# Performance work log

Hardware: AMD Instinct MI355X
Metric: run time of the kernel (lower is better)

## Reference

```python
import jax, jax.numpy as jnp
import numpy as np

IN_FEATURES = 8
OUT_FEATURES = 64
UNI_DEG = 3
INT_DEG = 3
N_ROWS = 500000


def _exponents():
    # Replicates the torch module's comb construction + filtering.
    deg = np.arange(UNI_DEG + 1)
    comb = np.array(np.meshgrid(*([deg] * IN_FEATURES))).T.reshape(-1, IN_FEATURES)
    s = comb.sum(axis=1)
    nz = (comb != 0).sum(axis=1)
    keep = ((nz == 1) & (s <= UNI_DEG)) | ((nz > 1) & (s <= INT_DEG))
    return comb[keep].astype(np.int32)  # [T, F] exponent matrix, T = 164


_E = _exponents()
NUM_TERMS = _E.shape[0]  # 164


def setup_inputs() -> dict:
    key = jax.random.key(0)
    kx, kw, kb = jax.random.split(key, 3)
    x = jax.random.normal(kx, (N_ROWS, IN_FEATURES), dtype=jnp.float32)
    weight = jax.random.normal(kw, (OUT_FEATURES, NUM_TERMS), dtype=jnp.float32) / np.sqrt(NUM_TERMS).astype(np.float32)
    bias = jax.random.normal(kb, (OUT_FEATURES,), dtype=jnp.float32) * 0.01
    return {"x": x, "weight": weight, "bias": bias}


def _poly_basis(x):
    # Power table pows[n, f, d] = x[n, f] ** d for d in 0..UNI_DEG.
    # Built with cumprod (exact integer powers, safe for negative x).
    xr = jnp.repeat(x[..., None], UNI_DEG, axis=-1)           # [N, F, UNI_DEG]
    pows = jnp.concatenate(
        [jnp.ones_like(x)[..., None], jnp.cumprod(xr, axis=-1)], axis=-1
    )                                                          # [N, F, UNI_DEG+1]
    E = jnp.asarray(_E)                                        # [T, F] int32
    basis = jnp.ones((x.shape[0], NUM_TERMS), x.dtype)
    for f in range(IN_FEATURES):  # small fixed loop over features
        basis = basis * pows[:, f, :][:, E[:, f]]              # gather -> [N, T]
    return basis


def reference(x, weight, bias):
    basis = _poly_basis(x)                                     # [N, T]
    return basis @ weight.T + bias                             # [N, out_features]
```

## Files before the change

kernel.cpp:

```cpp
#include <hip/hip_runtime.h>

#define NUM_ROWS 500000
#define TERMS 164
#define KSTEPS 6
#define NFRAG (KSTEPS * 4)
#define NITER ((NUM_ROWS + 63) / 64)
#define SOSTRIDE 68

typedef __attribute__((ext_vector_type(8))) short bf16x8;
typedef __attribute__((ext_vector_type(4))) float f32x4;
typedef __attribute__((ext_vector_type(4))) unsigned int uint4v;

struct ETab { int e[192][8]; int n; };

constexpr ETab make_et() {
    ETab T{};
    for (int i = 0; i < 192; ++i)
        for (int f = 0; f < 8; ++f) T.e[i][f] = 0;
    T.n = 0;
    for (int a = 0; a <= 3; ++a)
     for (int b = 0; a + b <= 3; ++b)
      for (int c = 0; a + b + c <= 3; ++c)
       for (int d = 0; a + b + c + d <= 3; ++d)
        for (int e_ = 0; a + b + c + d + e_ <= 3; ++e_)
         for (int f_ = 0; a + b + c + d + e_ + f_ <= 3; ++f_)
          for (int g = 0; a + b + c + d + e_ + f_ + g <= 3; ++g)
           for (int h = 0; a + b + c + d + e_ + f_ + g + h <= 3; ++h) {
               int s = a + b + c + d + e_ + f_ + g + h;
               if (s >= 1) {
                   T.e[T.n][0] = g;  T.e[T.n][1] = h;
                   T.e[T.n][2] = f_; T.e[T.n][3] = e_;
                   T.e[T.n][4] = d;  T.e[T.n][5] = c;
                   T.e[T.n][6] = b;  T.e[T.n][7] = a;
                   ++T.n;
               }
           }
    return T;
}

static_assert(make_et().n == TERMS, "term count must be 164");
__device__ constexpr ETab ET = make_et();

__device__ __forceinline__ unsigned int pack2bf(float a, float b) {
    unsigned int ua = __float_as_uint(a), ub = __float_as_uint(b);
    ua = ua + 0x7fffu + ((ua >> 16) & 1u);
    ub = ub + 0x7fffu + ((ub >> 16) & 1u);
    return (ua >> 16) | (ub & 0xffff0000u);
}

__device__ __forceinline__ float term_val(int t, const float (&p1)[8],
                                          const float (&p2)[8],
                                          const float (&p3)[8]) {
    if (t > TERMS) return 0.f;
    if (t == TERMS) return 1.f;
    float v = 1.f;
#pragma unroll
    for (int f = 0; f < 8; ++f) {
        const int d = ET.e[t][f];
        if (d == 1) v *= p1[f];
        else if (d == 2) v *= p2[f];
        else if (d == 3) v *= p3[f];
    }
    return v;
}

__device__ __forceinline__ float wval(const float* __restrict__ w,
                                      const float* __restrict__ b,
                                      int j, int t) {
    if (t < TERMS) return w[j * TERMS + t];
    if (t == TERMS) return b[j];
    return 0.f;
}

__global__ __launch_bounds__(256) void pack_weights_kernel(
        const float* __restrict__ weight, const float* __restrict__ bias,
        unsigned int* __restrict__ wpack) {
    int idx = blockIdx.x * 256 + threadIdx.x;
    if (idx >= NFRAG * 256) return;
    int p    = idx >> 8;
    int lane = (idx >> 2) & 63;
    int dw   = idx & 3;
    int ks = p >> 2, ct = p & 3;
    int kq = lane >> 4;
    int j  = (ct << 4) | (lane & 15);
    int t0 = ks * 32 + kq * 8 + dw * 2;
    wpack[idx] = pack2bf(wval(weight, bias, j, t0), wval(weight, bias, j, t0 + 1));
}

__device__ __forceinline__ void poly_body(const float* __restrict__ x,
                                          const uint4v* __restrict__ bsrc,
                                          float* __restrict__ out,
                                          uint4v (&sT)[4][4][64],
                                          f32x4 (&sO4)[4][16 * SOSTRIDE / 4]) {
    const int tid  = threadIdx.x;
    const int lane = tid & 63;
    const int wid  = tid >> 6;
    const int m    = lane & 15;
    const int kq   = lane >> 4;

    const int gw = blockIdx.x * 4 + wid;
    const int nw = gridDim.x * 4;

    float* sO = (float*)&sO4[wid][0];

    for (int it = gw; it < NITER; it += nw) {
        const int rbase = it * 64;
        const int myrow = rbase + lane;

        float4 xa = {0.f, 0.f, 0.f, 0.f}, xb = {0.f, 0.f, 0.f, 0.f};
        if (myrow < NUM_ROWS) {
            const float4* xp = (const float4*)(x + (size_t)myrow * 8);
            xa = xp[0]; xb = xp[1];
        }
        float p1[8], p2[8], p3[8];
        p1[0] = xa.x; p1[1] = xa.y; p1[2] = xa.z; p1[3] = xa.w;
        p1[4] = xb.x; p1[5] = xb.y; p1[6] = xb.z; p1[7] = xb.w;
#pragma unroll
        for (int f = 0; f < 8; ++f) {
            p2[f] = p1[f] * p1[f];
            p3[f] = p2[f] * p1[f];
        }

        f32x4 acc[4][4];
#pragma unroll
        for (int ct = 0; ct < 4; ++ct)
#pragma unroll
            for (int q = 0; q < 4; ++q)
                acc[ct][q] = (f32x4){0.f, 0.f, 0.f, 0.f};

#pragma unroll
        for (int ks = 0; ks < KSTEPS; ++ks) {
#pragma unroll
            for (int c = 0; c < 4; ++c) {
                uint4v ch;
#pragma unroll
                for (int d = 0; d < 4; ++d) {
                    float a = term_val(ks * 32 + c * 8 + d * 2,     p1, p2, p3);
                    float b = term_val(ks * 32 + c * 8 + d * 2 + 1, p1, p2, p3);
                    ch[d] = pack2bf(a, b);
                }
                sT[wid][c][lane] = ch;
            }

            uint4v aw[4];
#pragma unroll
            for (int ct = 0; ct < 4; ++ct)
                aw[ct] = bsrc[(ks * 4 + ct) * 64 + lane];

#pragma unroll
            for (int q = 0; q < 4; ++q) {
                uint4v bw = sT[wid][kq][q * 16 + m];
                bf16x8 bfrag = __builtin_bit_cast(bf16x8, bw);
#pragma unroll
                for (int ct = 0; ct < 4; ++ct) {
                    bf16x8 afrag = __builtin_bit_cast(bf16x8, aw[ct]);
                    acc[ct][q] = __builtin_amdgcn_mfma_f32_16x16x32_bf16(
                                     afrag, bfrag, acc[ct][q], 0, 0, 0);
                }
            }
        }

#pragma unroll
        for (int q = 0; q < 4; ++q) {
#pragma unroll
            for (int ct = 0; ct < 4; ++ct) {
                f32x4* pw = (f32x4*)(sO + m * SOSTRIDE + ct * 16 + kq * 4);
                *pw = acc[ct][q];
            }
#pragma unroll
            for (int g = 0; g < 4; ++g) {
                const int R = 4 * g + kq;
                f32x4 v = *(const f32x4*)(sO + R * SOSTRIDE + m * 4);
                const int orow = rbase + q * 16 + R;
                if (orow < NUM_ROWS) {
                    f32x4* po = (f32x4*)(out + (size_t)orow * 64 + m * 4);
                    *po = v;
                }
            }
        }
    }
}

__global__ __launch_bounds__(256) void poly_ws_kernel(
        const float* __restrict__ x, const unsigned int* __restrict__ wpack,
        float* __restrict__ out) {
    __shared__ uint4v sT[4][4][64];
    __shared__ f32x4  sO4[4][16 * SOSTRIDE / 4];
    poly_body(x, (const uint4v*)wpack, out, sT, sO4);
}

__global__ __launch_bounds__(256) void poly_lds_kernel(
        const float* __restrict__ x, const float* __restrict__ weight,
        const float* __restrict__ bias, float* __restrict__ out) {
    __shared__ uint4v sT[4][4][64];
    __shared__ f32x4  sO4[4][16 * SOSTRIDE / 4];
    __shared__ unsigned int sB[NFRAG * 256];
    const int tid = threadIdx.x;
#pragma unroll 1
    for (int idx = tid; idx < NFRAG * 256; idx += 256) {
        int p = idx >> 8, lane = (idx >> 2) & 63, dw = idx & 3;
        int ks = p >> 2, ct = p & 3, kq = lane >> 4;
        int j  = (ct << 4) | (lane & 15);
        int t0 = ks * 32 + kq * 8 + dw * 2;
        sB[idx] = pack2bf(wval(weight, bias, j, t0), wval(weight, bias, j, t0 + 1));
    }
    __syncthreads();
    poly_body(x, (const uint4v*)sB, out, sT, sO4);
}

extern "C" void kernel_launch(void* const* d_in, const int* in_sizes, int n_in,
                              void* d_out, int out_size, void* d_ws, size_t ws_size,
                              hipStream_t stream) {
    const float* x      = (const float*)d_in[0];
    const float* weight = (const float*)d_in[1];
    const float* bias   = (const float*)d_in[2];
    float* out          = (float*)d_out;

    if (ws_size >= (size_t)(NFRAG * 256 * sizeof(unsigned int))) {
        unsigned int* wpack = (unsigned int*)d_ws;
        pack_weights_kernel<<<NFRAG, 256, 0, stream>>>(weight, bias, wpack);
        poly_ws_kernel<<<2048, 256, 0, stream>>>(x, wpack, out);
    } else {
        poly_lds_kernel<<<1024, 256, 0, stream>>>(x, weight, bias, out);
    }
}
```

Before: 37.04 us.

## Prefetch next x tile, alias per-wave LDS buffers, halve grid size

The x rows for the next iteration are now loaded before the current tile is computed, so global-load latency overlaps the basis computation and MFMAs. The per-wave term buffer and output staging buffer share one LDS region, which shrinks LDS per block. Weight fragments are loaded inside the MFMA loop instead of being hoisted, which cuts register pressure. The grid drops from 2048 to 1024 blocks so each wave runs more iterations and the prefetch has more to hide. Aliasing the two buffers relies on in-wave ordering between the last sT read and the first sO write, and the smaller grid may lower occupancy-driven latency hiding.

```diff
diff --git a/kernel.cpp b/kernel.cpp
--- a/kernel.cpp
+++ b/kernel.cpp
@@ -6,6 +6,7 @@
 #define NFRAG (KSTEPS * 4)
 #define NITER ((NUM_ROWS + 63) / 64)
 #define SOSTRIDE 68
+#define WAVE_BYTES 4608
 
 typedef __attribute__((ext_vector_type(8))) short bf16x8;
 typedef __attribute__((ext_vector_type(4))) float f32x4;
@@ -87,31 +88,43 @@
     wpack[idx] = pack2bf(wval(weight, bias, j, t0), wval(weight, bias, j, t0 + 1));
 }
 
+__device__ __forceinline__ void load_x(const float* __restrict__ x, int myrow,
+                                       float4& xa, float4& xb) {
+    xa = {0.f, 0.f, 0.f, 0.f}; xb = {0.f, 0.f, 0.f, 0.f};
+    if (myrow < NUM_ROWS) {
+        const float4* xp = (const float4*)(x + (size_t)myrow * 8);
+        xa = xp[0]; xb = xp[1];
+    }
+}
+
 __device__ __forceinline__ void poly_body(const float* __restrict__ x,
                                           const uint4v* __restrict__ bsrc,
                                           float* __restrict__ out,
-                                          uint4v (&sT)[4][4][64],
-                                          f32x4 (&sO4)[4][16 * SOSTRIDE / 4]) {
+                                          char* __restrict__ smem) {
     const int tid  = threadIdx.x;
     const int lane = tid & 63;
     const int wid  = tid >> 6;
     const int m    = lane & 15;
     const int kq   = lane >> 4;
 
+    char* wbase = smem + wid * WAVE_BYTES;
+    uint4v* sT = (uint4v*)wbase;
+    float*  sO = (float*)wbase;
+
     const int gw = blockIdx.x * 4 + wid;
     const int nw = gridDim.x * 4;
 
-    float* sO = (float*)&sO4[wid][0];
-
-    for (int it = gw; it < NITER; it += nw) {
+    int it = gw;
+    float4 xa, xb;
+    if (it < NITER) load_x(x, it * 64 + lane, xa, xb);
+
+#pragma unroll 1
+    for (; it < NITER; ) {
+        const int itn = it + nw;
+        float4 xa2, xb2;
+        if (itn < NITER) load_x(x, itn * 64 + lane, xa2, xb2);
+
         const int rbase = it * 64;
-        const int myrow = rbase + lane;
-
-        float4 xa = {0.f, 0.f, 0.f, 0.f}, xb = {0.f, 0.f, 0.f, 0.f};
-        if (myrow < NUM_ROWS) {
-            const float4* xp = (const float4*)(x + (size_t)myrow * 8);
-            xa = xp[0]; xb = xp[1];
-        }
         float p1[8], p2[8], p3[8];
         p1[0] = xa.x; p1[1] = xa.y; p1[2] = xa.z; p1[3] = xa.w;
         p1[4] = xb.x; p1[5] = xb.y; p1[6] = xb.z; p1[7] = xb.w;
@@ -139,21 +152,17 @@
                     float b = term_val(ks * 32 + c * 8 + d * 2 + 1, p1, p2, p3);
                     ch[d] = pack2bf(a, b);
                 }
-                sT[wid][c][lane] = ch;
-            }
-
-            uint4v aw[4];
-#pragma unroll
-            for (int ct = 0; ct < 4; ++ct)
-                aw[ct] = bsrc[(ks * 4 + ct) * 64 + lane];
+                sT[c * 64 + lane] = ch;
+            }
 
 #pragma unroll
             for (int q = 0; q < 4; ++q) {
-                uint4v bw = sT[wid][kq][q * 16 + m];
+                uint4v bw = sT[kq * 64 + q * 16 + m];
                 bf16x8 bfrag = __builtin_bit_cast(bf16x8, bw);
 #pragma unroll
                 for (int ct = 0; ct < 4; ++ct) {
-                    bf16x8 afrag = __builtin_bit_cast(bf16x8, aw[ct]);
+                    uint4v aw = bsrc[(ks * 4 + ct) * 64 + lane];
+                    bf16x8 afrag = __builtin_bit_cast(bf16x8, aw);
                     acc[ct][q] = __builtin_amdgcn_mfma_f32_16x16x32_bf16(
                                      afrag, bfrag, acc[ct][q], 0, 0, 0);
                 }
@@ -178,22 +187,23 @@
                 }
             }
         }
+
+        xa = xa2; xb = xb2;
+        it = itn;
     }
 }
 
 __global__ __launch_bounds__(256) void poly_ws_kernel(
         const float* __restrict__ x, const unsigned int* __restrict__ wpack,
         float* __restrict__ out) {
-    __shared__ uint4v sT[4][4][64];
-    __shared__ f32x4  sO4[4][16 * SOSTRIDE / 4];
-    poly_body(x, (const uint4v*)wpack, out, sT, sO4);
+    __shared__ __align__(16) char smem[4 * WAVE_BYTES];
+    poly_body(x, (const uint4v*)wpack, out, smem);
 }
 
 __global__ __launch_bounds__(256) void poly_lds_kernel(
         const float* __restrict__ x, const float* __restrict__ weight,
         const float* __restrict__ bias, float* __restrict__ out) {
-    __shared__ uint4v sT[4][4][64];
-    __shared__ f32x4  sO4[4][16 * SOSTRIDE / 4];
+    __shared__ __align__(16) char smem[4 * WAVE_BYTES];
     __shared__ unsigned int sB[NFRAG * 256];
     const int tid = threadIdx.x;
 #pragma unroll 1
@@ -205,7 +215,7 @@
         sB[idx] = pack2bf(wval(weight, bias, j, t0), wval(weight, bias, j, t0 + 1));
     }
     __syncthreads();
-    poly_body(x, (const uint4v*)sB, out, sT, sO4);
+    poly_body(x, (const uint4v*)sB, out, smem);
 }
 
 extern "C" void kernel_launch(void* const* d_in, const int* in_sizes, int n_in,
@@ -219,7 +229,7 @@
     if (ws_size >= (size_t)(NFRAG * 256 * sizeof(unsigned int))) {
         unsigned int* wpack = (unsigned int*)d_ws;
         pack_weights_kernel<<<NFRAG, 256, 0, stream>>>(weight, bias, wpack);
-        poly_ws_kernel<<<2048, 256, 0, stream>>>(x, wpack, out);
+        poly_ws_kernel<<<1024, 256, 0, stream>>>(x, wpack, out);
     } else {
         poly_lds_kernel<<<1024, 256, 0, stream>>>(x, weight, bias, out);
     }
```

Result: slower. 38.50 us (+3.9%).
